# Kernel optimization log

Hardware: AMD Instinct MI355X
Metric: run time of the kernel (lower is better)

Reference implementation:

```python
import jax, jax.numpy as jnp
import numpy as np

D_MODEL = 1024
D_STATE = 16
D_CONV = 4
EXPAND = 2
NUM_LAYERS = 2
SEQ = 1024
BATCH = 2
D_INNER = EXPAND * D_MODEL          # 2048
DT_RANK = (D_MODEL + 15) // 16      # 64 (math.ceil(d_model/16))


def setup_inputs() -> dict:
    key = jax.random.key(0)
    ks = jax.random.split(key, 10)
    s = 0.02
    # A initialized as in mamba_ssm: A = repeat(arange(1, d_state+1), d_inner) -> A_log = log(A)
    A_log = jnp.log(jnp.broadcast_to(
        jnp.arange(1, D_STATE + 1, dtype=jnp.float32), (NUM_LAYERS, D_INNER, D_STATE)))
    return {
        "pe": jax.random.normal(ks[0], (SEQ, D_MODEL), jnp.float32) * s,
        "condition": jax.random.normal(ks[1], (BATCH, SEQ, D_MODEL), jnp.float32),
        "W_in": jax.random.normal(ks[2], (NUM_LAYERS, 2 * D_INNER, D_MODEL), jnp.float32) * s,
        "conv_w": jax.random.normal(ks[3], (NUM_LAYERS, D_INNER, D_CONV), jnp.float32) * s,
        "conv_b": jnp.zeros((NUM_LAYERS, D_INNER), jnp.float32),
        "W_x": jax.random.normal(ks[4], (NUM_LAYERS, DT_RANK + 2 * D_STATE, D_INNER), jnp.float32) * s,
        "W_dt": jax.random.normal(ks[5], (NUM_LAYERS, D_INNER, DT_RANK), jnp.float32) * s,
        "b_dt": jax.random.normal(ks[6], (NUM_LAYERS, D_INNER), jnp.float32) * s,
        "A_log": A_log,
        "Dp": jnp.ones((NUM_LAYERS, D_INNER), jnp.float32),
        "W_out": jax.random.normal(ks[7], (NUM_LAYERS, D_MODEL, D_INNER), jnp.float32) * s,
        "output_shape": BATCH,
    }


def _mamba_block(x, W_in, conv_w, conv_b, W_x, W_dt, b_dt, A_log, Dp, W_out):
    # x: [B, L, d_model]
    B, L, _ = x.shape
    xz = jnp.einsum('bld,ed->ble', x, W_in)          # [B, L, 2*d_inner]
    u, z = jnp.split(xz, 2, axis=-1)                 # each [B, L, d_inner]
    # causal depthwise conv1d (padding=d_conv-1, truncate to L)
    xp = jnp.pad(u, ((0, 0), (D_CONV - 1, 0), (0, 0)))
    xc = conv_b + sum(conv_w[:, k] * xp[:, k:k + L, :] for k in range(D_CONV))
    xc = jax.nn.silu(xc)                             # [B, L, d_inner]
    x_dbl = jnp.einsum('bld,ed->ble', xc, W_x)       # [B, L, dt_rank + 2*d_state]
    dt, Bm, Cm = jnp.split(x_dbl, [DT_RANK, DT_RANK + D_STATE], axis=-1)
    delta = jax.nn.softplus(jnp.einsum('blr,dr->bld', dt, W_dt) + b_dt)  # [B, L, d_inner]
    A = -jnp.exp(A_log)                              # [d_inner, d_state]

    def step(h, inputs):
        u_t, d_t, B_t, C_t = inputs                  # [B,di],[B,di],[B,ds],[B,ds]
        dA = jnp.exp(d_t[:, :, None] * A)            # [B, di, ds]
        h = dA * h + (d_t * u_t)[:, :, None] * B_t[:, None, :]
        y = jnp.einsum('bds,bs->bd', h, C_t)
        return h, y

    h0 = jnp.zeros((B, D_INNER, D_STATE), x.dtype)
    xs = (xc.transpose(1, 0, 2), delta.transpose(1, 0, 2),
          Bm.transpose(1, 0, 2), Cm.transpose(1, 0, 2))
    _, ys = jax.lax.scan(step, h0, xs)               # ys: [L, B, d_inner]
    y = ys.transpose(1, 0, 2) + xc * Dp
    out = y * jax.nn.silu(z)
    return jnp.einsum('bld,ed->ble', out, W_out)     # [B, L, d_model]


def reference(pe, condition, W_in, conv_w, conv_b, W_x, W_dt, b_dt, A_log, Dp, W_out, output_shape):
    # pe.repeat(B,1,1) + condition
    x = pe[None, :, :] + condition
    for i in range(NUM_LAYERS):
        x = _mamba_block(x, W_in[i], conv_w[i], conv_b[i], W_x[i],
                         W_dt[i], b_dt[i], A_log[i], Dp[i], W_out[i])
    return x
```

## Files before the change

### kernel.cpp

```cpp
#include <hip/hip_runtime.h>
#include <math.h>

#define D_MODEL 1024
#define D_INNER 2048
#define D_STATE 16
#define DT_RANK 64
#define SEQ 1024
#define BATCH 2
#define NLAYERS 2
#define ROWS (BATCH*SEQ)
#define XDIM 96
#define XZLD (2*D_INNER)

#define NC 32
#define CL 32
#define SDB 256

#define G2_ROWS 64
#define G2_KC 128
#define G2_BK 32
#define G2_KS (D_INNER / G2_KC)

typedef short bf16x8 __attribute__((ext_vector_type(8)));
typedef float f32x4  __attribute__((ext_vector_type(4)));

__device__ __forceinline__ unsigned short f2bf(float f) {
    union { float f; unsigned int u; } v; v.f = f;
    unsigned int u = v.u;
    return (unsigned short)((u + 0x7FFFu + ((u >> 16) & 1u)) >> 16);
}
__device__ __forceinline__ float bf2f(unsigned short u) {
    union { unsigned int i; float f; } v; v.i = ((unsigned int)u) << 16; return v.f;
}

__device__ __forceinline__ void gload_lds16(const void* g, void* s) {
    __builtin_amdgcn_global_load_lds((const __attribute__((address_space(1))) void*)g,
                                     (__attribute__((address_space(3))) void*)s, 16, 0, 0);
}

#define POW_TREE(E, e1)                                                         \
    E[0] = e1;          E[1] = e1 * e1;   E[2] = E[1] * e1;  E[3] = E[1] * E[1];\
    E[4] = E[3] * E[0]; E[5] = E[3] * E[1]; E[6] = E[3] * E[2]; E[7] = E[3] * E[3];\
    E[8] = E[7] * E[0]; E[9] = E[7] * E[1]; E[10] = E[7] * E[2]; E[11] = E[7] * E[3];\
    E[12] = E[7] * E[4]; E[13] = E[7] * E[5]; E[14] = E[7] * E[6]; E[15] = E[7] * E[7];

__global__ __launch_bounds__(256) void add_pe_kernel(const float* __restrict__ pe,
    const float* __restrict__ cond, float* __restrict__ X)
{
    int i = blockIdx.x * 256 + threadIdx.x;
    int total = ROWS * D_MODEL / 4;
    if (i >= total) return;
    int row  = i / (D_MODEL / 4);
    int l    = row & (SEQ - 1);
    int col4 = i - row * (D_MODEL / 4);
    float4 p = reinterpret_cast<const float4*>(pe)[l * (D_MODEL / 4) + col4];
    float4 c = reinterpret_cast<const float4*>(cond)[i];
    float4 r; r.x = p.x + c.x; r.y = p.y + c.y; r.z = p.z + c.z; r.w = p.w + c.w;
    reinterpret_cast<float4*>(X)[i] = r;
}

__global__ __launch_bounds__(256) void conv_bf16_dense(const float* __restrict__ src,
    unsigned short* __restrict__ dst, int n4)
{
    int i = blockIdx.x * 256 + threadIdx.x;
    if (i >= n4) return;
    float4 v = reinterpret_cast<const float4*>(src)[i];
    ushort4 o; o.x = f2bf(v.x); o.y = f2bf(v.y); o.z = f2bf(v.z); o.w = f2bf(v.w);
    reinterpret_cast<ushort4*>(dst)[i] = o;
}

#define WN1 (NLAYERS * 2 * D_INNER * D_MODEL / 4)
#define WN2 (NLAYERS * D_MODEL * D_INNER / 4)
#define WN3 (NLAYERS * D_INNER * DT_RANK / 4)
#define WN4 (ROWS * D_MODEL / 4)
__global__ __launch_bounds__(256) void conv_wall(const float* __restrict__ Win,
    const float* __restrict__ Wout, const float* __restrict__ Wdt,
    const float* __restrict__ pe, const float* __restrict__ cond,
    unsigned short* __restrict__ WINbf, unsigned short* __restrict__ WOUTbf,
    unsigned short* __restrict__ WDTbf, unsigned short* __restrict__ Xbf)
{
    int i = blockIdx.x * 256 + threadIdx.x;
    if (i < WN1) {
        float4 v = reinterpret_cast<const float4*>(Win)[i];
        ushort4 o; o.x = f2bf(v.x); o.y = f2bf(v.y); o.z = f2bf(v.z); o.w = f2bf(v.w);
        reinterpret_cast<ushort4*>(WINbf)[i] = o;
    } else if (i < WN1 + WN2) {
        int j = i - WN1;
        float4 v = reinterpret_cast<const float4*>(Wout)[j];
        ushort4 o; o.x = f2bf(v.x); o.y = f2bf(v.y); o.z = f2bf(v.z); o.w = f2bf(v.w);
        reinterpret_cast<ushort4*>(WOUTbf)[j] = o;
    } else if (i < WN1 + WN2 + WN3) {
        int j = i - WN1 - WN2;
        float4 v = reinterpret_cast<const float4*>(Wdt)[j];
        ushort4 o; o.x = f2bf(v.x); o.y = f2bf(v.y); o.z = f2bf(v.z); o.w = f2bf(v.w);
        reinterpret_cast<ushort4*>(WDTbf)[j] = o;
    } else if (i < WN1 + WN2 + WN3 + WN4) {
        int j = i - WN1 - WN2 - WN3;
        int row  = j / (D_MODEL / 4);
        int l    = row & (SEQ - 1);
        int col4 = j - row * (D_MODEL / 4);
        float4 p = reinterpret_cast<const float4*>(pe)[l * (D_MODEL / 4) + col4];
        float4 c = reinterpret_cast<const float4*>(cond)[j];
        ushort4 o;
        o.x = f2bf(p.x + c.x); o.y = f2bf(p.y + c.y);
        o.z = f2bf(p.z + c.z); o.w = f2bf(p.w + c.w);
        reinterpret_cast<ushort4*>(Xbf)[j] = o;
    }
}

__global__ __launch_bounds__(256) void conv_bf16_strided(const float* __restrict__ src,
    int ld, int cols, unsigned short* __restrict__ dst, int total4)
{
    int i = blockIdx.x * 256 + threadIdx.x;
    if (i >= total4) return;
    int c4  = cols / 4;
    int row = i / c4;
    int col = (i - row * c4) * 4;
    float4 v = *reinterpret_cast<const float4*>(src + (size_t)row * ld + col);
    ushort4 o; o.x = f2bf(v.x); o.y = f2bf(v.y); o.z = f2bf(v.z); o.w = f2bf(v.w);
    *reinterpret_cast<ushort4*>(dst + (size_t)row * cols + col) = o;
}

__global__ __launch_bounds__(256) void conv_bf16_dtcols(const float* __restrict__ XDBL,
    unsigned short* __restrict__ dst)
{
    int i = blockIdx.x * 256 + threadIdx.x;
    if (i >= ROWS * DT_RANK / 4) return;
    int m  = i >> 4;
    int c4 = (i & 15) * 4;
    float4 v = *reinterpret_cast<const float4*>(XDBL + (size_t)m * XDIM + c4);
    ushort4 o; o.x = f2bf(v.x); o.y = f2bf(v.y); o.z = f2bf(v.z); o.w = f2bf(v.w);
    *reinterpret_cast<ushort4*>(dst + (size_t)m * DT_RANK + c4) = o;
}

#define GBM 128
#define GBN 128
#define GBK 64

#define GEMM_STAGE(Ap, Bp, lda, ldb, koff)                                      \
    _Pragma("unroll")                                                           \
    for (int i_ = 0; i_ < 4; ++i_) {                                            \
        int off_ = w * 4096 + i_ * 1024 + l * 16;                               \
        int row_ = off_ >> 7;                                                   \
        int col_ = (off_ & 127) >> 1;                                           \
        gload_lds16(Ap + (size_t)(m0 + row_) * (lda) + (koff) + col_,           \
                    (char*)As + w * 4096 + i_ * 1024);                          \
    }                                                                           \
    _Pragma("unroll")                                                           \
    for (int i_ = 0; i_ < 4; ++i_) {                                            \
        int off_ = w * 4096 + i_ * 1024 + l * 16;                               \
        int row_ = off_ >> 7;                                                   \
        int col_ = (off_ & 127) >> 1;                                           \
        gload_lds16(Bp + (size_t)(n0 + row_) * (ldb) + (koff) + col_,           \
                    (char*)Bs + w * 4096 + i_ * 1024);                          \
    }

#define GEMM_MFMA_STEP                                                          \
    _Pragma("unroll")                                                           \
    for (int kk = 0; kk < 2; ++kk) {                                            \
        bf16x8 af[4], bfr[4];                                                   \
        _Pragma("unroll")                                                       \
        for (int m = 0; m < 4; ++m)                                             \
            af[m] = *(const bf16x8*)&As[(wr * 64 + m * 16 + fr) * GBK + kk * 32 + fq * 8]; \
        _Pragma("unroll")                                                       \
        for (int n = 0; n < 4; ++n)                                             \
            bfr[n] = *(const bf16x8*)&Bs[(wc * 64 + n * 16 + fr) * GBK + kk * 32 + fq * 8]; \
        _Pragma("unroll")                                                       \
        for (int m = 0; m < 4; ++m)                                             \
            _Pragma("unroll")                                                   \
            for (int n = 0; n < 4; ++n)                                         \
                acc[m][n] = __builtin_amdgcn_mfma_f32_16x16x32_bf16(af[m], bfr[n], acc[m][n], 0, 0, 0); \
    }

__global__ __launch_bounds__(256) void gemm_bf16_nt(const unsigned short* __restrict__ A,
    const unsigned short* __restrict__ B, float* __restrict__ C,
    int M, int N, int K, int ldc, const float* __restrict__ bias, int epilogue)
{
    __shared__ unsigned short As[GBM * GBK];
    __shared__ unsigned short Bs[GBN * GBK];
    int tid = threadIdx.x;
    int w = tid >> 6, l = tid & 63;
    int wr = w >> 1, wc = w & 1;
    int m0 = blockIdx.y * GBM, n0 = blockIdx.x * GBN;

    f32x4 acc[4][4];
    #pragma unroll
    for (int m = 0; m < 4; ++m)
        #pragma unroll
        for (int n = 0; n < 4; ++n) acc[m][n] = (f32x4){0.f, 0.f, 0.f, 0.f};
    int fr = l & 15, fq = l >> 4;

    for (int k0 = 0; k0 < K; k0 += GBK) {
        GEMM_STAGE(A, B, K, K, k0)
        __syncthreads();
        GEMM_MFMA_STEP
        __syncthreads();
    }

    #pragma unroll
    for (int m = 0; m < 4; ++m)
        #pragma unroll
        for (int n = 0; n < 4; ++n) {
            int col = n0 + wc * 64 + n * 16 + fr;
            #pragma unroll
            for (int j = 0; j < 4; ++j) {
                int row = m0 + wr * 64 + m * 16 + fq * 4 + j;
                float v = acc[m][n][j];
                if (epilogue == 1) {
                    v += bias[col];
                    v = fmaxf(v, 0.f) + log1pf(__expf(-fabsf(v)));
                }
                C[(size_t)row * ldc + col] = v;
            }
        }
}

__global__ __launch_bounds__(256) void gemm_bf16_nt_bfout(const unsigned short* __restrict__ A,
    const unsigned short* __restrict__ B, unsigned short* __restrict__ C,
    int M, int N, int K, int ldc)
{
    __shared__ unsigned short As[GBM * GBK];
    __shared__ unsigned short Bs[GBN * GBK];
    int tid = threadIdx.x;
    int w = tid >> 6, l = tid & 63;
    int wr = w >> 1, wc = w & 1;
    int m0 = blockIdx.y * GBM, n0 = blockIdx.x * GBN;

    f32x4 acc[4][4];
    #pragma unroll
    for (int m = 0; m < 4; ++m)
        #pragma unroll
        for (int n = 0; n < 4; ++n) acc[m][n] = (f32x4){0.f, 0.f, 0.f, 0.f};
    int fr = l & 15, fq = l >> 4;

    for (int k0 = 0; k0 < K; k0 += GBK) {
        GEMM_STAGE(A, B, K, K, k0)
        __syncthreads();
        GEMM_MFMA_STEP
        __syncthreads();
    }

    #pragma unroll
    for (int m = 0; m < 4; ++m)
        #pragma unroll
        for (int n = 0; n < 4; ++n) {
            int col = n0 + wc * 64 + n * 16 + fr;
            #pragma unroll
            for (int j = 0; j < 4; ++j) {
                int row = m0 + wr * 64 + m * 16 + fq * 4 + j;
                C[(size_t)row * ldc + col] = f2bf(acc[m][n][j]);
            }
        }
}

__global__ __launch_bounds__(256) void gemm_bf16_sp_bfout(const unsigned short* __restrict__ A,
    const unsigned short* __restrict__ B, unsigned short* __restrict__ C,
    int M, int N, int K, int ldc, const float* __restrict__ bias)
{
    __shared__ unsigned short As[GBM * GBK];
    __shared__ unsigned short Bs[GBN * GBK];
    int tid = threadIdx.x;
    int w = tid >> 6, l = tid & 63;
    int wr = w >> 1, wc = w & 1;
    int m0 = blockIdx.y * GBM, n0 = blockIdx.x * GBN;

    f32x4 acc[4][4];
    #pragma unroll
    for (int m = 0; m < 4; ++m)
        #pragma unroll
        for (int n = 0; n < 4; ++n) acc[m][n] = (f32x4){0.f, 0.f, 0.f, 0.f};
    int fr = l & 15, fq = l >> 4;

    for (int k0 = 0; k0 < K; k0 += GBK) {
        GEMM_STAGE(A, B, K, K, k0)
        __syncthreads();
        GEMM_MFMA_STEP
        __syncthreads();
    }

    #pragma unroll
    for (int m = 0; m < 4; ++m)
        #pragma unroll
        for (int n = 0; n < 4; ++n) {
            int col = n0 + wc * 64 + n * 16 + fr;
            float bv = bias[col];
            #pragma unroll
            for (int j = 0; j < 4; ++j) {
                int row = m0 + wr * 64 + m * 16 + fq * 4 + j;
                float v = acc[m][n][j] + bv;
                v = fmaxf(v, 0.f) + log1pf(__expf(-fabsf(v)));
                C[(size_t)row * ldc + col] = f2bf(v);
            }
        }
}

__global__ __launch_bounds__(256) void gemm_bf16_nt_ks(const unsigned short* __restrict__ A, int lda,
    const unsigned short* __restrict__ B, int ldb, float* __restrict__ P,
    int M, int N, int Kper)
{
    __shared__ unsigned short As[GBM * GBK];
    __shared__ unsigned short Bs[GBN * GBK];
    int tid = threadIdx.x;
    int w = tid >> 6, l = tid & 63;
    int wr = w >> 1, wc = w & 1;
    int m0 = blockIdx.y * GBM, n0 = blockIdx.x * GBN;
    int koff = blockIdx.z * Kper;
    float* Pz = P + (size_t)blockIdx.z * M * N;

    f32x4 acc[4][4];
    #pragma unroll
    for (int m = 0; m < 4; ++m)
        #pragma unroll
        for (int n = 0; n < 4; ++n) acc[m][n] = (f32x4){0.f, 0.f, 0.f, 0.f};
    int fr = l & 15, fq = l >> 4;

    for (int k0 = 0; k0 < Kper; k0 += GBK) {
        GEMM_STAGE(A, B, lda, ldb, koff + k0)
        __syncthreads();
        GEMM_MFMA_STEP
        __syncthreads();
    }

    #pragma unroll
    for (int m = 0; m < 4; ++m)
        #pragma unroll
        for (int n = 0; n < 4; ++n) {
            int col = n0 + wc * 64 + n * 16 + fr;
            #pragma unroll
            for (int j = 0; j < 4; ++j) {
                int row = m0 + wr * 64 + m * 16 + fq * 4 + j;
                Pz[(size_t)row * N + col] = acc[m][n][j];
            }
        }
}

__global__ __launch_bounds__(256) void gemm4_reduce(const float* __restrict__ P,
    float* __restrict__ X, unsigned short* __restrict__ Xbf)
{
    int i = blockIdx.x * 256 + threadIdx.x;
    if (i >= ROWS * D_MODEL / 4) return;
    float4 a = reinterpret_cast<const float4*>(P)[i];
    float4 b = reinterpret_cast<const float4*>(P + (size_t)ROWS * D_MODEL)[i];
    float4 r; r.x = a.x + b.x; r.y = a.y + b.y; r.z = a.z + b.z; r.w = a.w + b.w;
    if (X) reinterpret_cast<float4*>(X)[i] = r;
    if (Xbf) {
        ushort4 o; o.x = f2bf(r.x); o.y = f2bf(r.y); o.z = f2bf(r.z); o.w = f2bf(r.w);
        reinterpret_cast<ushort4*>(Xbf)[i] = o;
    }
}

__global__ __launch_bounds__(256) void gemm2_fused(const unsigned short* __restrict__ XZbf,
    const float* __restrict__ cw, const float* __restrict__ cb,
    const float* __restrict__ B, unsigned short* __restrict__ XCbf,
    float* __restrict__ P)
{
    __shared__ float Axc[G2_KC][68];
    __shared__ float Bs[G2_BK][XDIM + 1];
    int tid = threadIdx.x;
    int m0 = blockIdx.x * G2_ROWS;
    int kc = blockIdx.y;
    int k0 = kc * G2_KC;

    {
        int d_loc = tid & 127;
        int d     = k0 + d_loc;
        int r0    = m0 + (tid >> 7) * 32;
        float4 wv = *(const float4*)(cw + (size_t)d * 4);
        float cbv = cb[d];
        int l0 = r0 & (SEQ - 1);
        float u3 = (l0 >= 3) ? bf2f(XZbf[(size_t)(r0 - 3) * XZLD + d]) : 0.f;
        float u2 = (l0 >= 2) ? bf2f(XZbf[(size_t)(r0 - 2) * XZLD + d]) : 0.f;
        float u1 = (l0 >= 1) ? bf2f(XZbf[(size_t)(r0 - 1) * XZLD + d]) : 0.f;
        int rl0 = r0 - m0;
        #pragma unroll 4
        for (int t = 0; t < 32; ++t) {
            float u0 = bf2f(XZbf[(size_t)(r0 + t) * XZLD + d]);
            float v = cbv + wv.x * u3 + wv.y * u2 + wv.z * u1 + wv.w * u0;
            v = v / (1.f + __expf(-v));
            Axc[d_loc][rl0 + t] = v;
            XCbf[(size_t)(r0 + t) * D_INNER + d] = f2bf(v);
            u3 = u2; u2 = u1; u1 = u0;
        }
    }
    __syncthreads();

    int rg = tid >> 4;
    int cg = tid & 15;
    float acc[4][6];
    #pragma unroll
    for (int i = 0; i < 4; ++i)
        #pragma unroll
        for (int j = 0; j < 6; ++j) acc[i][j] = 0.f;

    for (int kb = 0; kb < G2_KC; kb += G2_BK) {
        {
            #pragma unroll
            for (int i = 0; i < 3; ++i) {
                int idx = tid + i * 256;
                int col = idx >> 3;
                int kk  = (idx & 7) * 4;
                float4 v = *(const float4*)(B + (size_t)col * D_INNER + k0 + kb + kk);
                Bs[kk + 0][col] = v.x;
                Bs[kk + 1][col] = v.y;
                Bs[kk + 2][col] = v.z;
                Bs[kk + 3][col] = v.w;
            }
        }
        __syncthreads();
        #pragma unroll
        for (int k = 0; k < G2_BK; ++k) {
            float4 a  = *(const float4*)&Axc[kb + k][rg * 4];
            float2 b0 = *(const float2*)&Bs[k][cg * 6];
            float2 b1 = *(const float2*)&Bs[k][cg * 6 + 2];
            float2 b2 = *(const float2*)&Bs[k][cg * 6 + 4];
            float av[4] = {a.x, a.y, a.z, a.w};
            float bv[6] = {b0.x, b0.y, b1.x, b1.y, b2.x, b2.y};
            #pragma unroll
            for (int i = 0; i < 4; ++i)
                #pragma unroll
                for (int j = 0; j < 6; ++j) acc[i][j] += av[i] * bv[j];
        }
        __syncthreads();
    }

    #pragma unroll
    for (int i = 0; i < 4; ++i)
        #pragma unroll
        for (int j = 0; j < 6; ++j)
            P[((size_t)kc * ROWS + m0 + rg * 4 + i) * XDIM + cg * 6 + j] = acc[i][j];
}

__global__ __launch_bounds__(256) void gemm2_splitk(const float* __restrict__ A,
    const float* __restrict__ B, float* __restrict__ P)
{
    __shared__ float As[G2_BK][G2_ROWS];
    __shared__ float Bs[G2_BK][XDIM + 1];
    int tid = threadIdx.x;
    int m0 = blockIdx.x * G2_ROWS;
    int kc = blockIdx.y;
    int k0 = kc * G2_KC;

    int rg = tid >> 4;
    int cg = tid & 15;
    float acc[4][6];
    #pragma unroll
    for (int i = 0; i < 4; ++i)
        #pragma unroll
        for (int j = 0; j < 6; ++j) acc[i][j] = 0.f;

    for (int kb = 0; kb < G2_KC; kb += G2_BK) {
        {
            int row = tid & 63;
            int kk  = (tid >> 6) * 4;
            #pragma unroll
            for (int i = 0; i < 2; ++i) {
                float4 v = *(const float4*)(A + (size_t)(m0 + row) * D_INNER + k0 + kb + kk + i * 16);
                As[kk + i * 16 + 0][row] = v.x;
                As[kk + i * 16 + 1][row] = v.y;
                As[kk + i * 16 + 2][row] = v.z;
                As[kk + i * 16 + 3][row] = v.w;
            }
        }
        {
            #pragma unroll
            for (int i = 0; i < 3; ++i) {
                int idx = tid + i * 256;
                int col = idx >> 3;
                int kk  = (idx & 7) * 4;
                float4 v = *(const float4*)(B + (size_t)col * D_INNER + k0 + kb + kk);
                Bs[kk + 0][col] = v.x;
                Bs[kk + 1][col] = v.y;
                Bs[kk + 2][col] = v.z;
                Bs[kk + 3][col] = v.w;
            }
        }
        __syncthreads();
        #pragma unroll
        for (int k = 0; k < G2_BK; ++k) {
            float4 a  = *(const float4*)&As[k][rg * 4];
            float2 b0 = *(const float2*)&Bs[k][cg * 6];
            float2 b1 = *(const float2*)&Bs[k][cg * 6 + 2];
            float2 b2 = *(const float2*)&Bs[k][cg * 6 + 4];
            float av[4] = {a.x, a.y, a.z, a.w};
            float bv[6] = {b0.x, b0.y, b1.x, b1.y, b2.x, b2.y};
            #pragma unroll
            for (int i = 0; i < 4; ++i)
                #pragma unroll
                for (int j = 0; j < 6; ++j) acc[i][j] += av[i] * bv[j];
        }
        __syncthreads();
    }

    #pragma unroll
    for (int i = 0; i < 4; ++i)
        #pragma unroll
        for (int j = 0; j < 6; ++j)
            P[((size_t)kc * ROWS + m0 + rg * 4 + i) * XDIM + cg * 6 + j] = acc[i][j];
}

__global__ __launch_bounds__(256) void gemm2_reduce(const float* __restrict__ P,
    float* __restrict__ XDBLo, unsigned short* __restrict__ dtbf)
{
    int i = blockIdx.x * 256 + threadIdx.x;
    if (i >= ROWS * XDIM / 4) return;
    float4 acc = make_float4(0.f, 0.f, 0.f, 0.f);
    #pragma unroll
    for (int ks = 0; ks < G2_KS; ++ks) {
        float4 v = *(const float4*)(P + (size_t)ks * ROWS * XDIM + (size_t)i * 4);
        acc.x += v.x; acc.y += v.y; acc.z += v.z; acc.w += v.w;
    }
    *(float4*)(XDBLo + (size_t)i * 4) = acc;
    if (dtbf) {
        int row = (i * 4) / XDIM;
        int col = (i * 4) - row * XDIM;
        if (col < DT_RANK) {
            ushort4 o; o.x = f2bf(acc.x); o.y = f2bf(acc.y); o.z = f2bf(acc.z); o.w = f2bf(acc.w);
            *reinterpret_cast<ushort4*>(dtbf + (size_t)row * DT_RANK + col) = o;
        }
    }
}

#define BM 64
#define BN 64
#define BK 16
__global__ __launch_bounds__(256) void gemm_nt(const float* __restrict__ A, int lda,
                                               const float* __restrict__ B, int ldb,
                                               float* __restrict__ C, int ldc,
                                               int M, int N, int K,
                                               const float* __restrict__ bias, int epilogue)
{
    __shared__ float As[BM][BK + 1];
    __shared__ float Bs[BN][BK + 1];
    int t  = threadIdx.x;
    int m0 = blockIdx.y * BM;
    int n0 = blockIdx.x * BN;
    int lrow = t >> 2;
    int lk   = (t & 3) * 4;
    int tm   = t >> 4;
    int tn   = t & 15;

    float acc[4][4];
    #pragma unroll
    for (int i = 0; i < 4; ++i)
        #pragma unroll
        for (int j = 0; j < 4; ++j) acc[i][j] = 0.f;

    for (int k0 = 0; k0 < K; k0 += BK) {
        {
            int row = m0 + lrow;
            float4 v = make_float4(0.f, 0.f, 0.f, 0.f);
            if (row < M) v = *reinterpret_cast<const float4*>(A + (size_t)row * lda + k0 + lk);
            As[lrow][lk + 0] = v.x; As[lrow][lk + 1] = v.y;
            As[lrow][lk + 2] = v.z; As[lrow][lk + 3] = v.w;
        }
        {
            int row = n0 + lrow;
            float4 v = make_float4(0.f, 0.f, 0.f, 0.f);
            if (row < N) v = *reinterpret_cast<const float4*>(B + (size_t)row * ldb + k0 + lk);
            Bs[lrow][lk + 0] = v.x; Bs[lrow][lk + 1] = v.y;
            Bs[lrow][lk + 2] = v.z; Bs[lrow][lk + 3] = v.w;
        }
        __syncthreads();
        #pragma unroll
        for (int kk = 0; kk < BK; ++kk) {
            float a[4], b[4];
            #pragma unroll
            for (int i = 0; i < 4; ++i) a[i] = As[tm * 4 + i][kk];
            #pragma unroll
            for (int j = 0; j < 4; ++j) b[j] = Bs[tn * 4 + j][kk];
            #pragma unroll
            for (int i = 0; i < 4; ++i)
                #pragma unroll
                for (int j = 0; j < 4; ++j) acc[i][j] += a[i] * b[j];
        }
        __syncthreads();
    }

    #pragma unroll
    for (int i = 0; i < 4; ++i) {
        int m = m0 + tm * 4 + i;
        if (m >= M) continue;
        #pragma unroll
        for (int j = 0; j < 4; ++j) {
            int n = n0 + tn * 4 + j;
            if (n >= N) continue;
            float v = acc[i][j];
            if (epilogue == 1) {
                v += bias[n];
                v = fmaxf(v, 0.f) + log1pf(__expf(-fabsf(v)));
            }
            C[(size_t)m * ldc + n] = v;
        }
    }
}

__global__ __launch_bounds__(256) void conv_silu_kernel(const float* __restrict__ XZ,
    const float* __restrict__ cw, const float* __restrict__ cb, float* __restrict__ XC)
{
    int idx = blockIdx.x * 256 + threadIdx.x;
    if (idx >= ROWS * (D_INNER / 4)) return;
    int d4   = idx % (D_INNER / 4);
    int rl   = idx / (D_INNER / 4);
    int l    = rl & (SEQ - 1);
    int base = rl - l;
    int d    = d4 * 4;

    float4 acc = reinterpret_cast<const float4*>(cb)[d4];
    float w[4][4];
    #pragma unroll
    for (int dd = 0; dd < 4; ++dd) {
        float4 wv = *reinterpret_cast<const float4*>(cw + (size_t)(d + dd) * 4);
        w[dd][0] = wv.x; w[dd][1] = wv.y; w[dd][2] = wv.z; w[dd][3] = wv.w;
    }
    #pragma unroll
    for (int k = 0; k < 4; ++k) {
        int lr = l - 3 + k;
        if (lr < 0) continue;
        float4 u = *reinterpret_cast<const float4*>(XZ + (size_t)(base + lr) * XZLD + d);
        acc.x += w[0][k] * u.x; acc.y += w[1][k] * u.y;
        acc.z += w[2][k] * u.z; acc.w += w[3][k] * u.w;
    }
    acc.x = acc.x / (1.f + __expf(-acc.x));
    acc.y = acc.y / (1.f + __expf(-acc.y));
    acc.z = acc.z / (1.f + __expf(-acc.z));
    acc.w = acc.w / (1.f + __expf(-acc.w));
    reinterpret_cast<float4*>(XC)[idx] = acc;
}


__global__ __launch_bounds__(SDB) void scan_part1b(const unsigned short* __restrict__ XCbf,
    const unsigned short* __restrict__ DL, const float* __restrict__ XDBL,
    const float* __restrict__ A_log, float* __restrict__ Psum, float* __restrict__ Ssum)
{
    __shared__ float sB[CL][16];
    int tid = threadIdx.x;
    int d = blockIdx.x * SDB + tid;
    int c = blockIdx.y, b = blockIdx.z;
    size_t r0 = (size_t)b * SEQ + (size_t)c * CL;

    if (tid < CL * 4) {
        int t = tid >> 2, j = (tid & 3) * 4;
        *(float4*)&sB[t][j] = *(const float4*)(XDBL + (r0 + t) * XDIM + DT_RANK + j);
    }

    float a[D_STATE], S[D_STATE];
    #pragma unroll
    for (int i = 0; i < 4; ++i) {
        float4 v = *(const float4*)(A_log + (size_t)d * D_STATE + i * 4);
        a[i*4+0] = -__expf(v.x); a[i*4+1] = -__expf(v.y);
        a[i*4+2] = -__expf(v.z); a[i*4+3] = -__expf(v.w);
    }
    bool powok = true;
    #pragma unroll
    for (int s = 0; s < D_STATE; ++s)
        powok = powok && (fabsf(a[s] + (float)(s + 1)) < 1e-3f * (float)(s + 1));
    #pragma unroll
    for (int s = 0; s < D_STATE; ++s) S[s] = 0.f;
    float sumdl = 0.f;
    __syncthreads();

    if (powok) {
        for (int t = 0; t < CL; ++t) {
            float dl = bf2f(DL[(r0 + t) * D_INNER + d]);
            float uu = bf2f(XCbf[(r0 + t) * D_INNER + d]);
            float du = dl * uu;
            sumdl += dl;
            float4 b0 = *(const float4*)&sB[t][0];
            float4 b1 = *(const float4*)&sB[t][4];
            float4 b2 = *(const float4*)&sB[t][8];
            float4 b3 = *(const float4*)&sB[t][12];
            float bv[16] = {b0.x,b0.y,b0.z,b0.w, b1.x,b1.y,b1.z,b1.w,
                            b2.x,b2.y,b2.z,b2.w, b3.x,b3.y,b3.z,b3.w};
            float e1 = __expf(-dl);
            float E[16];
            POW_TREE(E, e1)
            #pragma unroll
            for (int s = 0; s < D_STATE; ++s)
                S[s] = E[s] * S[s] + du * bv[s];
        }
    } else {
        for (int t = 0; t < CL; ++t) {
            float dl = bf2f(DL[(r0 + t) * D_INNER + d]);
            float uu = bf2f(XCbf[(r0 + t) * D_INNER + d]);
            float du = dl * uu;
            sumdl += dl;
            float4 b0 = *(const float4*)&sB[t][0];
            float4 b1 = *(const float4*)&sB[t][4];
            float4 b2 = *(const float4*)&sB[t][8];
            float4 b3 = *(const float4*)&sB[t][12];
            float bv[16] = {b0.x,b0.y,b0.z,b0.w, b1.x,b1.y,b1.z,b1.w,
                            b2.x,b2.y,b2.z,b2.w, b3.x,b3.y,b3.z,b3.w};
            #pragma unroll
            for (int s = 0; s < D_STATE; ++s) {
                float e = __expf(dl * a[s]);
                S[s] = e * S[s] + du * bv[s];
            }
        }
    }

    size_t o = (((size_t)b * NC + c) * D_INNER + d) * D_STATE;
    #pragma unroll
    for (int i = 0; i < 4; ++i) {
        float4 p, s4;
        p.x = __expf(a[i*4+0] * sumdl); p.y = __expf(a[i*4+1] * sumdl);
        p.z = __expf(a[i*4+2] * sumdl); p.w = __expf(a[i*4+3] * sumdl);
        s4.x = S[i*4+0]; s4.y = S[i*4+1]; s4.z = S[i*4+2]; s4.w = S[i*4+3];
        *(float4*)(Psum + o + i * 4) = p;
        *(float4*)(Ssum + o + i * 4) = s4;
    }
}

__global__ __launch_bounds__(256) void scan_prefix(float* __restrict__ Psum,
    const float* __restrict__ Ssum)
{
    int idx = blockIdx.x * 256 + threadIdx.x;
    int b = idx >> 15;
    int rem = idx & 32767;
    float h = 0.f;
    for (int c = 0; c < NC; ++c) {
        size_t o = (((size_t)b * NC + c) * D_INNER * D_STATE) + rem;
        float p = Psum[o];
        float s = Ssum[o];
        Psum[o] = h;
        h = p * h + s;
    }
}

__global__ __launch_bounds__(SDB) void scan_part2b(const unsigned short* __restrict__ XCbf,
    unsigned short* __restrict__ DL, const unsigned short* __restrict__ XZbf,
    const float* __restrict__ XDBL, const float* __restrict__ A_log,
    const float* __restrict__ Dp, const float* __restrict__ Hin)
{
    __shared__ float sBC[CL][32];
    int tid = threadIdx.x;
    int d = blockIdx.x * SDB + tid;
    int c = blockIdx.y, b = blockIdx.z;
    size_t r0 = (size_t)b * SEQ + (size_t)c * CL;

    {
        int t = tid >> 3, j = (tid & 7) * 4;
        *(float4*)&sBC[t][j] = *(const float4*)(XDBL + (r0 + t) * XDIM + DT_RANK + j);
    }

    float a[D_STATE], h[D_STATE];
    #pragma unroll
    for (int i = 0; i < 4; ++i) {
        float4 v = *(const float4*)(A_log + (size_t)d * D_STATE + i * 4);
        a[i*4+0] = -__expf(v.x); a[i*4+1] = -__expf(v.y);
        a[i*4+2] = -__expf(v.z); a[i*4+3] = -__expf(v.w);
    }
    bool powok = true;
    #pragma unroll
    for (int s = 0; s < D_STATE; ++s)
        powok = powok && (fabsf(a[s] + (float)(s + 1)) < 1e-3f * (float)(s + 1));
    size_t ho = (((size_t)b * NC + c) * D_INNER + d) * D_STATE;
    #pragma unroll
    for (int i = 0; i < 4; ++i) {
        float4 v = *(const float4*)(Hin + ho + i * 4);
        h[i*4+0] = v.x; h[i*4+1] = v.y; h[i*4+2] = v.z; h[i*4+3] = v.w;
    }
    float dp = Dp[d];
    __syncthreads();

    if (powok) {
        for (int t = 0; t < CL; ++t) {
            float dl = bf2f(DL[(r0 + t) * D_INNER + d]);
            float uu = bf2f(XCbf[(r0 + t) * D_INNER + d]);
            float z  = bf2f(XZbf[(r0 + t) * XZLD + D_INNER + d]);
            float du = dl * uu;
            float4 b0 = *(const float4*)&sBC[t][0];
            float4 b1 = *(const float4*)&sBC[t][4];
            float4 b2 = *(const float4*)&sBC[t][8];
            float4 b3 = *(const float4*)&sBC[t][12];
            float4 c0 = *(const float4*)&sBC[t][16];
            float4 c1 = *(const float4*)&sBC[t][20];
            float4 c2 = *(const float4*)&sBC[t][24];
            float4 c3 = *(const float4*)&sBC[t][28];
            float bv[16] = {b0.x,b0.y,b0.z,b0.w, b1.x,b1.y,b1.z,b1.w,
                            b2.x,b2.y,b2.z,b2.w, b3.x,b3.y,b3.z,b3.w};
            float cv[16] = {c0.x,c0.y,c0.z,c0.w, c1.x,c1.y,c1.z,c1.w,
                            c2.x,c2.y,c2.z,c2.w, c3.x,c3.y,c3.z,c3.w};
            float e1 = __expf(-dl);
            float E[16];
            POW_TREE(E, e1)
            float y = 0.f;
            #pragma unroll
            for (int s = 0; s < D_STATE; ++s) {
                h[s] = E[s] * h[s] + du * bv[s];
                y += h[s] * cv[s];
            }
            float sz = z / (1.f + __expf(-z));
            DL[(r0 + t) * D_INNER + d] = f2bf((y + uu * dp) * sz);
        }
    } else {
        for (int t = 0; t < CL; ++t) {
            float dl = bf2f(DL[(r0 + t) * D_INNER + d]);
            float uu = bf2f(XCbf[(r0 + t) * D_INNER + d]);
            float z  = bf2f(XZbf[(r0 + t) * XZLD + D_INNER + d]);
            float du = dl * uu;
            float4 b0 = *(const float4*)&sBC[t][0];
            float4 b1 = *(const float4*)&sBC[t][4];
            float4 b2 = *(const float4*)&sBC[t][8];
            float4 b3 = *(const float4*)&sBC[t][12];
            float4 c0 = *(const float4*)&sBC[t][16];
            float4 c1 = *(const float4*)&sBC[t][20];
            float4 c2 = *(const float4*)&sBC[t][24];
            float4 c3 = *(const float4*)&sBC[t][28];
            float bv[16] = {b0.x,b0.y,b0.z,b0.w, b1.x,b1.y,b1.z,b1.w,
                            b2.x,b2.y,b2.z,b2.w, b3.x,b3.y,b3.z,b3.w};
            float cv[16] = {c0.x,c0.y,c0.z,c0.w, c1.x,c1.y,c1.z,c1.w,
                            c2.x,c2.y,c2.z,c2.w, c3.x,c3.y,c3.z,c3.w};
            float y = 0.f;
            #pragma unroll
            for (int s = 0; s < D_STATE; ++s) {
                float e = __expf(dl * a[s]);
                h[s] = e * h[s] + du * bv[s];
                y += h[s] * cv[s];
            }
            float sz = z / (1.f + __expf(-z));
            DL[(r0 + t) * D_INNER + d] = f2bf((y + uu * dp) * sz);
        }
    }
}

__global__ __launch_bounds__(SDB) void scan_part1(const float* __restrict__ XC,
    const float* __restrict__ XZ, const float* __restrict__ XDBL,
    const float* __restrict__ A_log, float* __restrict__ Psum, float* __restrict__ Ssum)
{
    __shared__ float sB[CL][16];
    int tid = threadIdx.x;
    int d = blockIdx.x * SDB + tid;
    int c = blockIdx.y, b = blockIdx.z;
    size_t r0 = (size_t)b * SEQ + (size_t)c * CL;

    if (tid < CL * 4) {
        int t = tid >> 2, j = (tid & 3) * 4;
        *(float4*)&sB[t][j] = *(const float4*)(XDBL + (r0 + t) * XDIM + DT_RANK + j);
    }

    float a[D_STATE], S[D_STATE];
    #pragma unroll
    for (int i = 0; i < 4; ++i) {
        float4 v = *(const float4*)(A_log + (size_t)d * D_STATE + i * 4);
        a[i*4+0] = -__expf(v.x); a[i*4+1] = -__expf(v.y);
        a[i*4+2] = -__expf(v.z); a[i*4+3] = -__expf(v.w);
    }
    #pragma unroll
    for (int s = 0; s < D_STATE; ++s) S[s] = 0.f;
    float sumdl = 0.f;
    __syncthreads();

    for (int t = 0; t < CL; ++t) {
        float dl = XZ[(r0 + t) * XZLD + d];
        float uu = XC[(r0 + t) * D_INNER + d];
        float du = dl * uu;
        sumdl += dl;
        float4 b0 = *(const float4*)&sB[t][0];
        float4 b1 = *(const float4*)&sB[t][4];
        float4 b2 = *(const float4*)&sB[t][8];
        float4 b3 = *(const float4*)&sB[t][12];
        float bv[16] = {b0.x,b0.y,b0.z,b0.w, b1.x,b1.y,b1.z,b1.w,
                        b2.x,b2.y,b2.z,b2.w, b3.x,b3.y,b3.z,b3.w};
        #pragma unroll
        for (int s = 0; s < D_STATE; ++s) {
            float e = __expf(dl * a[s]);
            S[s] = e * S[s] + du * bv[s];
        }
    }

    size_t o = (((size_t)b * NC + c) * D_INNER + d) * D_STATE;
    #pragma unroll
    for (int i = 0; i < 4; ++i) {
        float4 p, s4;
        p.x = __expf(a[i*4+0] * sumdl); p.y = __expf(a[i*4+1] * sumdl);
        p.z = __expf(a[i*4+2] * sumdl); p.w = __expf(a[i*4+3] * sumdl);
        s4.x = S[i*4+0]; s4.y = S[i*4+1]; s4.z = S[i*4+2]; s4.w = S[i*4+3];
        *(float4*)(Psum + o + i * 4) = p;
        *(float4*)(Ssum + o + i * 4) = s4;
    }
}

__global__ __launch_bounds__(SDB) void scan_part2(const float* __restrict__ XC,
    float* __restrict__ XZ, const float* __restrict__ XDBL,
    const float* __restrict__ A_log, const float* __restrict__ Dp,
    const float* __restrict__ Hin)
{
    __shared__ float sBC[CL][32];
    int tid = threadIdx.x;
    int d = blockIdx.x * SDB + tid;
    int c = blockIdx.y, b = blockIdx.z;
    size_t r0 = (size_t)b * SEQ + (size_t)c * CL;

    {
        int t = tid >> 3, j = (tid & 7) * 4;
        *(float4*)&sBC[t][j] = *(const float4*)(XDBL + (r0 + t) * XDIM + DT_RANK + j);
    }

    float a[D_STATE], h[D_STATE];
    #pragma unroll
    for (int i = 0; i < 4; ++i) {
        float4 v = *(const float4*)(A_log + (size_t)d * D_STATE + i * 4);
        a[i*4+0] = -__expf(v.x); a[i*4+1] = -__expf(v.y);
        a[i*4+2] = -__expf(v.z); a[i*4+3] = -__expf(v.w);
    }
    size_t ho = (((size_t)b * NC + c) * D_INNER + d) * D_STATE;
    #pragma unroll
    for (int i = 0; i < 4; ++i) {
        float4 v = *(const float4*)(Hin + ho + i * 4);
        h[i*4+0] = v.x; h[i*4+1] = v.y; h[i*4+2] = v.z; h[i*4+3] = v.w;
    }
    float dp = Dp[d];
    __syncthreads();

    for (int t = 0; t < CL; ++t) {
        float dl = XZ[(r0 + t) * XZLD + d];
        float uu = XC[(r0 + t) * D_INNER + d];
        float z  = XZ[(r0 + t) * XZLD + D_INNER + d];
        float du = dl * uu;
        float4 b0 = *(const float4*)&sBC[t][0];
        float4 b1 = *(const float4*)&sBC[t][4];
        float4 b2 = *(const float4*)&sBC[t][8];
        float4 b3 = *(const float4*)&sBC[t][12];
        float4 c0 = *(const float4*)&sBC[t][16];
        float4 c1 = *(const float4*)&sBC[t][20];
        float4 c2 = *(const float4*)&sBC[t][24];
        float4 c3 = *(const float4*)&sBC[t][28];
        float bv[16] = {b0.x,b0.y,b0.z,b0.w, b1.x,b1.y,b1.z,b1.w,
                        b2.x,b2.y,b2.z,b2.w, b3.x,b3.y,b3.z,b3.w};
        float cv[16] = {c0.x,c0.y,c0.z,c0.w, c1.x,c1.y,c1.z,c1.w,
                        c2.x,c2.y,c2.z,c2.w, c3.x,c3.y,c3.z,c3.w};
        float y = 0.f;
        #pragma unroll
        for (int s = 0; s < D_STATE; ++s) {
            float e = __expf(dl * a[s]);
            h[s] = e * h[s] + du * bv[s];
            y += h[s] * cv[s];
        }
        float sz = z / (1.f + __expf(-z));
        XZ[(r0 + t) * XZLD + d] = (y + uu * dp) * sz;
    }
}

__global__ __launch_bounds__(256) void scan_kernel2(const float* __restrict__ XC,
    float* __restrict__ XZ, const float* __restrict__ XDBL,
    const float* __restrict__ A_log, const float* __restrict__ Dp)
{
    int tid = threadIdx.x;
    int s  = tid & 15;
    int dd = tid >> 4;
    int d  = blockIdx.x * 16 + dd;
    int b  = blockIdx.y;

    float a  = -__expf(A_log[(size_t)d * D_STATE + s]);
    float h  = 0.f;
    float dp = Dp[d];
    const size_t rbase = (size_t)b * SEQ;

    for (int t = 0; t < SEQ; ++t) {
        size_t r = rbase + t;
        float dl = XZ[r * XZLD + d];
        float uu = XC[r * D_INNER + d];
        float z  = XZ[r * XZLD + D_INNER + d];
        float Bv = XDBL[r * XDIM + DT_RANK + s];
        float Cv = XDBL[r * XDIM + DT_RANK + D_STATE + s];
        float e  = __expf(dl * a);
        h = e * h + dl * uu * Bv;
        float y = h * Cv;
        y += __shfl_xor(y, 1);
        y += __shfl_xor(y, 2);
        y += __shfl_xor(y, 4);
        y += __shfl_xor(y, 8);
        if (s == 0) {
            float sz = z / (1.f + __expf(-z));
            XZ[r * XZLD + d] = (y + uu * dp) * sz;
        }
    }
}

extern "C" void kernel_launch(void* const* d_in, const int* in_sizes, int n_in,
                              void* d_out, int out_size, void* d_ws, size_t ws_size,
                              hipStream_t stream)
{
    const float* pe    = (const float*)d_in[0];
    const float* cond  = (const float*)d_in[1];
    const float* W_in  = (const float*)d_in[2];
    const float* cw    = (const float*)d_in[3];
    const float* cb    = (const float*)d_in[4];
    const float* W_x   = (const float*)d_in[5];
    const float* W_dt  = (const float*)d_in[6];
    const float* b_dt  = (const float*)d_in[7];
    const float* A_log = (const float*)d_in[8];
    const float* Dp    = (const float*)d_in[9];
    const float* W_out = (const float*)d_in[10];

    float* X = (float*)d_out;

    char* wsp = (char*)d_ws;
    unsigned short* XZbf = (unsigned short*)wsp;
    unsigned short* XCbf = (unsigned short*)(wsp + 16777216);
    float* XDBL  = (float*)(wsp + 33554432);
    unsigned short* BF0   = (unsigned short*)(wsp + 34340864);
    unsigned short* dtbf  = (unsigned short*)(wsp + 42729472);
    unsigned short* WINbf = (unsigned short*)(wsp + 42991616);
    unsigned short* WOUTbf= (unsigned short*)(wsp + 59768832);
    unsigned short* WDTbf = (unsigned short*)(wsp + 68157440);
    float* SCR   = (float*)(wsp + 68681728);
    size_t need_A = 68681728 + 16777216;

    float* XZb   = (float*)d_ws;
    float* XCb   = XZb + (size_t)ROWS * XZLD;
    float* XDBLb = XCb + (size_t)ROWS * D_INNER;
    void* rest = (void*)(XDBLb + (size_t)ROWS * XDIM);
    unsigned short* Abf = (unsigned short*)rest;
    unsigned short* Bbf = Abf + (size_t)ROWS * D_INNER;
    float* PpartB = (float*)rest;
    float* PsumB  = (float*)rest;
    float* SsumB  = PsumB + (size_t)BATCH * NC * D_INNER * D_STATE;
    size_t need_B = ((size_t)ROWS * XZLD + (size_t)ROWS * D_INNER + (size_t)ROWS * XDIM) * 4
                  + ((size_t)ROWS * D_INNER + (size_t)ROWS * D_INNER) * 2;

    if (ws_size >= need_A) {
        float* Psum = SCR;
        float* Ssum = SCR + (size_t)BATCH * NC * D_INNER * D_STATE;

        conv_wall<<<(WN1 + WN2 + WN3 + WN4 + 255) / 256, 256, 0, stream>>>(
            W_in, W_out, W_dt, pe, cond, WINbf, WOUTbf, WDTbf, BF0);

        for (int l = 0; l < NLAYERS; ++l) {
            const unsigned short* WINl  = WINbf  + (size_t)l * 2 * D_INNER * D_MODEL;
            const unsigned short* WOUTl = WOUTbf + (size_t)l * D_MODEL * D_INNER;
            const unsigned short* WDTl  = WDTbf  + (size_t)l * D_INNER * DT_RANK;
            const float* W_x_l   = W_x   + (size_t)l * XDIM * D_INNER;
            const float* cw_l    = cw    + (size_t)l * D_INNER * 4;
            const float* cb_l    = cb    + (size_t)l * D_INNER;
            const float* b_dt_l  = b_dt  + (size_t)l * D_INNER;
            const float* A_log_l = A_log + (size_t)l * D_INNER * D_STATE;
            const float* Dp_l    = Dp    + (size_t)l * D_INNER;

            gemm_bf16_nt_bfout<<<dim3(2 * D_INNER / GBN, ROWS / GBM), 256, 0, stream>>>(
                BF0, WINl, XZbf, ROWS, 2 * D_INNER, D_MODEL, XZLD);
            gemm2_fused<<<dim3(ROWS / G2_ROWS, G2_KS), 256, 0, stream>>>(
                XZbf, cw_l, cb_l, W_x_l, XCbf, SCR);
            gemm2_reduce<<<(ROWS * XDIM / 4 + 255) / 256, 256, 0, stream>>>(SCR, XDBL, dtbf);
            gemm_bf16_sp_bfout<<<dim3(D_INNER / GBN, ROWS / GBM), 256, 0, stream>>>(
                dtbf, WDTl, BF0, ROWS, D_INNER, DT_RANK, D_INNER, b_dt_l);
            scan_part1b<<<dim3(D_INNER / SDB, NC, BATCH), SDB, 0, stream>>>(
                XCbf, BF0, XDBL, A_log_l, Psum, Ssum);
            scan_prefix<<<BATCH * D_INNER * D_STATE / 256, 256, 0, stream>>>(Psum, Ssum);
            scan_part2b<<<dim3(D_INNER / SDB, NC, BATCH), SDB, 0, stream>>>(
                XCbf, BF0, XZbf, XDBL, A_log_l, Dp_l, Psum);
            gemm_bf16_nt_ks<<<dim3(D_MODEL / GBN, ROWS / GBM, 2), 256, 0, stream>>>(
                BF0, D_INNER, WOUTl, D_INNER, SCR, ROWS, D_MODEL, D_INNER / 2);
            gemm4_reduce<<<(ROWS * D_MODEL / 4 + 255) / 256, 256, 0, stream>>>(
                SCR, (l == NLAYERS - 1) ? X : nullptr, (l < NLAYERS - 1) ? BF0 : nullptr);
        }
    } else if (ws_size >= need_B) {
        add_pe_kernel<<<ROWS * D_MODEL / 4 / 256, 256, 0, stream>>>(pe, cond, X);
        for (int l = 0; l < NLAYERS; ++l) {
            const float* W_in_l  = W_in  + (size_t)l * 2 * D_INNER * D_MODEL;
            const float* W_out_l = W_out + (size_t)l * D_MODEL * D_INNER;
            const float* W_x_l   = W_x   + (size_t)l * XDIM * D_INNER;
            const float* W_dt_l  = W_dt  + (size_t)l * D_INNER * DT_RANK;
            const float* b_dt_l  = b_dt  + (size_t)l * D_INNER;
            const float* A_log_l = A_log + (size_t)l * D_INNER * D_STATE;
            const float* Dp_l    = Dp    + (size_t)l * D_INNER;

            conv_bf16_dense<<<(ROWS * D_MODEL / 4 + 255) / 256, 256, 0, stream>>>(X, Abf, ROWS * D_MODEL / 4);
            conv_bf16_dense<<<(2 * D_INNER * D_MODEL / 4 + 255) / 256, 256, 0, stream>>>(W_in_l, Bbf, 2 * D_INNER * D_MODEL / 4);
            gemm_bf16_nt<<<dim3(2 * D_INNER / GBN, ROWS / GBM), 256, 0, stream>>>(
                Abf, Bbf, XZb, ROWS, 2 * D_INNER, D_MODEL, XZLD, nullptr, 0);
            conv_silu_kernel<<<ROWS * (D_INNER / 4) / 256, 256, 0, stream>>>(
                XZb, cw + (size_t)l * D_INNER * 4, cb + (size_t)l * D_INNER, XCb);
            gemm2_splitk<<<dim3(ROWS / G2_ROWS, G2_KS), 256, 0, stream>>>(XCb, W_x_l, PpartB);
            gemm2_reduce<<<(ROWS * XDIM / 4 + 255) / 256, 256, 0, stream>>>(PpartB, XDBLb, nullptr);
            conv_bf16_dtcols<<<(ROWS * DT_RANK / 4 + 255) / 256, 256, 0, stream>>>(XDBLb, Abf);
            conv_bf16_dense<<<(D_INNER * DT_RANK / 4 + 255) / 256, 256, 0, stream>>>(W_dt_l, Bbf, D_INNER * DT_RANK / 4);
            gemm_bf16_nt<<<dim3(D_INNER / GBN, ROWS / GBM), 256, 0, stream>>>(
                Abf, Bbf, XZb, ROWS, D_INNER, DT_RANK, XZLD, b_dt_l, 1);
            scan_part1<<<dim3(D_INNER / SDB, NC, BATCH), SDB, 0, stream>>>(
                XCb, XZb, XDBLb, A_log_l, PsumB, SsumB);
            scan_prefix<<<BATCH * D_INNER * D_STATE / 256, 256, 0, stream>>>(PsumB, SsumB);
            scan_part2<<<dim3(D_INNER / SDB, NC, BATCH), SDB, 0, stream>>>(
                XCb, XZb, XDBLb, A_log_l, Dp_l, PsumB);
            conv_bf16_strided<<<(ROWS * D_INNER / 4 + 255) / 256, 256, 0, stream>>>(
                XZb, XZLD, D_INNER, Abf, ROWS * D_INNER / 4);
            conv_bf16_dense<<<(D_MODEL * D_INNER / 4 + 255) / 256, 256, 0, stream>>>(W_out_l, Bbf, D_MODEL * D_INNER / 4);
            gemm_bf16_nt<<<dim3(D_MODEL / GBN, ROWS / GBM), 256, 0, stream>>>(
                Abf, Bbf, X, ROWS, D_MODEL, D_INNER, D_MODEL, nullptr, 0);
        }
    } else {
        add_pe_kernel<<<ROWS * D_MODEL / 4 / 256, 256, 0, stream>>>(pe, cond, X);
        for (int l = 0; l < NLAYERS; ++l) {
            gemm_nt<<<dim3(2 * D_INNER / BN, ROWS / BM), 256, 0, stream>>>(
                X, D_MODEL, W_in + (size_t)l * 2 * D_INNER * D_MODEL, D_MODEL,
                XZb, XZLD, ROWS, 2 * D_INNER, D_MODEL, nullptr, 0);
            conv_silu_kernel<<<ROWS * (D_INNER / 4) / 256, 256, 0, stream>>>(
                XZb, cw + (size_t)l * D_INNER * 4, cb + (size_t)l * D_INNER, XCb);
            gemm_nt<<<dim3((XDIM + BN - 1) / BN, ROWS / BM), 256, 0, stream>>>(
                XCb, D_INNER, W_x + (size_t)l * XDIM * D_INNER, D_INNER,
                XDBLb, XDIM, ROWS, XDIM, D_INNER, nullptr, 0);
            gemm_nt<<<dim3(D_INNER / BN, ROWS / BM), 256, 0, stream>>>(
                XDBLb, XDIM, W_dt + (size_t)l * D_INNER * DT_RANK, DT_RANK,
                XZb, XZLD, ROWS, D_INNER, DT_RANK, b_dt + (size_t)l * D_INNER, 1);
            scan_kernel2<<<dim3(D_INNER / 16, BATCH), 256, 0, stream>>>(
                XCb, XZb, XDBLb, A_log + (size_t)l * D_INNER * D_STATE, Dp + (size_t)l * D_INNER);
            gemm_nt<<<dim3(D_MODEL / BN, ROWS / BM), 256, 0, stream>>>(
                XZb, XZLD, W_out + (size_t)l * D_MODEL * D_INNER, D_INNER,
                X, D_MODEL, ROWS, D_MODEL, D_INNER, nullptr, 0);
        }
    }
}
```

Baseline: 321.3 us.

## Replace split-K out-projection GEMM with narrow-tile GEMM and lengthen scan chunks

The out-projection drops its split-K kernel and separate reduce kernel. A new GEMM with a 64-wide N tile covers the full K and writes bf16 or fp32 output directly, and the next layer reads the bf16 result from an aliased buffer. Separately, scan chunks change from 32×32 to 16 chunks of length 64, which halves the prefix state traffic but gives fewer blocks and longer sequential loops. The cost removed is the fp32 partial round-trip and one launch; the risk is lower parallelism in the GEMM's K loop and in the scan.

```diff
diff --git a/kernel.cpp b/kernel.cpp
--- a/kernel.cpp
+++ b/kernel.cpp
@@ -12,8 +12,8 @@
 #define XDIM 96
 #define XZLD (2*D_INNER)
 
-#define NC 32
-#define CL 32
+#define NC 16
+#define CL 64
 #define SDB 256
 
 #define G2_ROWS 64
@@ -294,59 +294,75 @@
         }
 }
 
-__global__ __launch_bounds__(256) void gemm_bf16_nt_ks(const unsigned short* __restrict__ A, int lda,
-    const unsigned short* __restrict__ B, int ldb, float* __restrict__ P,
-    int M, int N, int Kper)
+#define G4BN 64
+__global__ __launch_bounds__(256) void gemm_bf16_nt64(const unsigned short* __restrict__ A, int lda,
+    const unsigned short* __restrict__ B, int ldb,
+    unsigned short* __restrict__ Cbf, float* __restrict__ Cf,
+    int M, int N, int K)
 {
     __shared__ unsigned short As[GBM * GBK];
-    __shared__ unsigned short Bs[GBN * GBK];
+    __shared__ unsigned short Bs[G4BN * GBK];
     int tid = threadIdx.x;
     int w = tid >> 6, l = tid & 63;
     int wr = w >> 1, wc = w & 1;
-    int m0 = blockIdx.y * GBM, n0 = blockIdx.x * GBN;
-    int koff = blockIdx.z * Kper;
-    float* Pz = P + (size_t)blockIdx.z * M * N;
-
-    f32x4 acc[4][4];
+    int m0 = blockIdx.y * GBM, n0 = blockIdx.x * G4BN;
+
+    f32x4 acc[4][2];
     #pragma unroll
     for (int m = 0; m < 4; ++m)
         #pragma unroll
-        for (int n = 0; n < 4; ++n) acc[m][n] = (f32x4){0.f, 0.f, 0.f, 0.f};
+        for (int n = 0; n < 2; ++n) acc[m][n] = (f32x4){0.f, 0.f, 0.f, 0.f};
     int fr = l & 15, fq = l >> 4;
 
-    for (int k0 = 0; k0 < Kper; k0 += GBK) {
-        GEMM_STAGE(A, B, lda, ldb, koff + k0)
-        __syncthreads();
-        GEMM_MFMA_STEP
+    for (int k0 = 0; k0 < K; k0 += GBK) {
+        #pragma unroll
+        for (int i_ = 0; i_ < 4; ++i_) {
+            int off_ = w * 4096 + i_ * 1024 + l * 16;
+            int row_ = off_ >> 7;
+            int col_ = (off_ & 127) >> 1;
+            gload_lds16(A + (size_t)(m0 + row_) * lda + k0 + col_,
+                        (char*)As + w * 4096 + i_ * 1024);
+        }
+        #pragma unroll
+        for (int i_ = 0; i_ < 2; ++i_) {
+            int off_ = w * 2048 + i_ * 1024 + l * 16;
+            int row_ = off_ >> 7;
+            int col_ = (off_ & 127) >> 1;
+            gload_lds16(B + (size_t)(n0 + row_) * ldb + k0 + col_,
+                        (char*)Bs + w * 2048 + i_ * 1024);
+        }
+        __syncthreads();
+        #pragma unroll
+        for (int kk = 0; kk < 2; ++kk) {
+            bf16x8 af[4], bfr[2];
+            #pragma unroll
+            for (int m = 0; m < 4; ++m)
+                af[m] = *(const bf16x8*)&As[(wr * 64 + m * 16 + fr) * GBK + kk * 32 + fq * 8];
+            #pragma unroll
+            for (int n = 0; n < 2; ++n)
+                bfr[n] = *(const bf16x8*)&Bs[(wc * 32 + n * 16 + fr) * GBK + kk * 32 + fq * 8];
+            #pragma unroll
+            for (int m = 0; m < 4; ++m)
+                #pragma unroll
+                for (int n = 0; n < 2; ++n)
+                    acc[m][n] = __builtin_amdgcn_mfma_f32_16x16x32_bf16(af[m], bfr[n], acc[m][n], 0, 0, 0);
+        }
         __syncthreads();
     }
 
     #pragma unroll
     for (int m = 0; m < 4; ++m)
         #pragma unroll
-        for (int n = 0; n < 4; ++n) {
-            int col = n0 + wc * 64 + n * 16 + fr;
+        for (int n = 0; n < 2; ++n) {
+            int col = n0 + wc * 32 + n * 16 + fr;
             #pragma unroll
             for (int j = 0; j < 4; ++j) {
                 int row = m0 + wr * 64 + m * 16 + fq * 4 + j;
-                Pz[(size_t)row * N + col] = acc[m][n][j];
+                float v = acc[m][n][j];
+                if (Cbf) Cbf[(size_t)row * N + col] = f2bf(v);
+                else     Cf[(size_t)row * N + col] = v;
             }
         }
-}
-
-__global__ __launch_bounds__(256) void gemm4_reduce(const float* __restrict__ P,
-    float* __restrict__ X, unsigned short* __restrict__ Xbf)
-{
-    int i = blockIdx.x * 256 + threadIdx.x;
-    if (i >= ROWS * D_MODEL / 4) return;
-    float4 a = reinterpret_cast<const float4*>(P)[i];
-    float4 b = reinterpret_cast<const float4*>(P + (size_t)ROWS * D_MODEL)[i];
-    float4 r; r.x = a.x + b.x; r.y = a.y + b.y; r.z = a.z + b.z; r.w = a.w + b.w;
-    if (X) reinterpret_cast<float4*>(X)[i] = r;
-    if (Xbf) {
-        ushort4 o; o.x = f2bf(r.x); o.y = f2bf(r.y); o.z = f2bf(r.z); o.w = f2bf(r.w);
-        reinterpret_cast<ushort4*>(Xbf)[i] = o;
-    }
 }
 
 __global__ __launch_bounds__(256) void gemm2_fused(const unsigned short* __restrict__ XZbf,
@@ -638,8 +654,10 @@
     int c = blockIdx.y, b = blockIdx.z;
     size_t r0 = (size_t)b * SEQ + (size_t)c * CL;
 
-    if (tid < CL * 4) {
-        int t = tid >> 2, j = (tid & 3) * 4;
+    #pragma unroll
+    for (int i = 0; i < (CL * 4) / SDB; ++i) {
+        int idx = tid + i * SDB;
+        int t = idx >> 2, j = (idx & 3) * 4;
         *(float4*)&sB[t][j] = *(const float4*)(XDBL + (r0 + t) * XDIM + DT_RANK + j);
     }
 
@@ -737,8 +755,10 @@
     int c = blockIdx.y, b = blockIdx.z;
     size_t r0 = (size_t)b * SEQ + (size_t)c * CL;
 
-    {
-        int t = tid >> 3, j = (tid & 7) * 4;
+    #pragma unroll
+    for (int i = 0; i < (CL * 8) / SDB; ++i) {
+        int idx = tid + i * SDB;
+        int t = idx >> 3, j = (idx & 7) * 4;
         *(float4*)&sBC[t][j] = *(const float4*)(XDBL + (r0 + t) * XDIM + DT_RANK + j);
     }
 
@@ -833,8 +853,10 @@
     int c = blockIdx.y, b = blockIdx.z;
     size_t r0 = (size_t)b * SEQ + (size_t)c * CL;
 
-    if (tid < CL * 4) {
-        int t = tid >> 2, j = (tid & 3) * 4;
+    #pragma unroll
+    for (int i = 0; i < (CL * 4) / SDB; ++i) {
+        int idx = tid + i * SDB;
+        int t = idx >> 2, j = (idx & 3) * 4;
         *(float4*)&sB[t][j] = *(const float4*)(XDBL + (r0 + t) * XDIM + DT_RANK + j);
     }
 
@@ -891,8 +913,10 @@
     int c = blockIdx.y, b = blockIdx.z;
     size_t r0 = (size_t)b * SEQ + (size_t)c * CL;
 
-    {
-        int t = tid >> 3, j = (tid & 7) * 4;
+    #pragma unroll
+    for (int i = 0; i < (CL * 8) / SDB; ++i) {
+        int idx = tid + i * SDB;
+        int t = idx >> 3, j = (idx & 7) * 4;
         *(float4*)&sBC[t][j] = *(const float4*)(XDBL + (r0 + t) * XDIM + DT_RANK + j);
     }
 
@@ -998,6 +1022,7 @@
     char* wsp = (char*)d_ws;
     unsigned short* XZbf = (unsigned short*)wsp;
     unsigned short* XCbf = (unsigned short*)(wsp + 16777216);
+    unsigned short* XOUT = XCbf;
     float* XDBL  = (float*)(wsp + 33554432);
     unsigned short* BF0   = (unsigned short*)(wsp + 34340864);
     unsigned short* dtbf  = (unsigned short*)(wsp + 42729472);
@@ -1036,9 +1061,10 @@
             const float* b_dt_l  = b_dt  + (size_t)l * D_INNER;
             const float* A_log_l = A_log + (size_t)l * D_INNER * D_STATE;
             const float* Dp_l    = Dp    + (size_t)l * D_INNER;
+            const unsigned short* xin = (l == 0) ? BF0 : XOUT;
 
             gemm_bf16_nt_bfout<<<dim3(2 * D_INNER / GBN, ROWS / GBM), 256, 0, stream>>>(
-                BF0, WINl, XZbf, ROWS, 2 * D_INNER, D_MODEL, XZLD);
+                xin, WINl, XZbf, ROWS, 2 * D_INNER, D_MODEL, XZLD);
             gemm2_fused<<<dim3(ROWS / G2_ROWS, G2_KS), 256, 0, stream>>>(
                 XZbf, cw_l, cb_l, W_x_l, XCbf, SCR);
             gemm2_reduce<<<(ROWS * XDIM / 4 + 255) / 256, 256, 0, stream>>>(SCR, XDBL, dtbf);
@@ -1049,10 +1075,11 @@
             scan_prefix<<<BATCH * D_INNER * D_STATE / 256, 256, 0, stream>>>(Psum, Ssum);
             scan_part2b<<<dim3(D_INNER / SDB, NC, BATCH), SDB, 0, stream>>>(
                 XCbf, BF0, XZbf, XDBL, A_log_l, Dp_l, Psum);
-            gemm_bf16_nt_ks<<<dim3(D_MODEL / GBN, ROWS / GBM, 2), 256, 0, stream>>>(
-                BF0, D_INNER, WOUTl, D_INNER, SCR, ROWS, D_MODEL, D_INNER / 2);
-            gemm4_reduce<<<(ROWS * D_MODEL / 4 + 255) / 256, 256, 0, stream>>>(
-                SCR, (l == NLAYERS - 1) ? X : nullptr, (l < NLAYERS - 1) ? BF0 : nullptr);
+            gemm_bf16_nt64<<<dim3(D_MODEL / G4BN, ROWS / GBM), 256, 0, stream>>>(
+                BF0, D_INNER, WOUTl, D_INNER,
+                (l < NLAYERS - 1) ? XOUT : nullptr,
+                (l == NLAYERS - 1) ? X : nullptr,
+                ROWS, D_MODEL, D_INNER);
         }
     } else if (ws_size >= need_B) {
         add_pe_kernel<<<ROWS * D_MODEL / 4 / 256, 256, 0, stream>>>(pe, cond, X);
```

Result: slower. 361.5 us (+12.5%).
